# Kernel optimization log

Measured on AMD Instinct MI355X. Metric: run time of the kernel, lower is better.

Reference implementation:

```python
import jax, jax.numpy as jnp
import numpy as np

B, L, D, N, R = 8, 4096, 768, 16, 8

def setup_inputs() -> dict:
    key = jax.random.key(0)
    ks = jax.random.split(key, 12)
    return {
        "x": jax.random.normal(ks[0], (B, L, D), jnp.float32),
        "a_logit": jnp.zeros((N,), jnp.float32),
        "U": jax.random.normal(ks[1], (N, R), jnp.float32) * 0.02,
        "V": jax.random.normal(ks[2], (N, R), jnp.float32) * 0.02,
        "W_in": jax.random.normal(ks[3], (N, D), jnp.float32) * (1.0 / np.sqrt(D)),
        "b_in": jax.random.normal(ks[4], (N,), jnp.float32) * 0.02,
        "W_gate": jax.random.normal(ks[5], (N, D), jnp.float32) * (1.0 / np.sqrt(D)),
        "b_gate": jax.random.normal(ks[6], (N,), jnp.float32) * 0.02,
        "W_out": jax.random.normal(ks[7], (D, N), jnp.float32) * (1.0 / np.sqrt(N)),
        "b_out": jax.random.normal(ks[8], (D,), jnp.float32) * 0.02,
        "W_skip": jax.random.normal(ks[9], (D, D), jnp.float32) * (1.0 / np.sqrt(D)),
        "b_skip": jax.random.normal(ks[10], (D,), jnp.float32) * 0.02,
    }

def reference(x, a_logit, U, V, W_in, b_in, W_gate, b_gate, W_out, b_out, W_skip, b_skip):
    # x: [B, L, D]
    u = jnp.einsum('bld,nd->bln', x, W_in) + b_in            # [B, L, N]
    g = jax.nn.sigmoid(jnp.einsum('bld,nd->bln', x, W_gate) + b_gate)
    a = jax.nn.sigmoid(a_logit)                              # [N]
    lowrank_T = V @ U.T                                      # (U @ V.T).T, [N, N]
    gu = g * u                                               # [B, L, N]

    def step(h, gu_t):
        # h: [B, N]; h_new = a*h + g_t*u_t + h @ lowrank.T
        h = h * a + gu_t + h @ lowrank_T
        return h, h

    h0 = jnp.zeros((x.shape[0], a_logit.shape[0]), x.dtype)
    _, hs = jax.lax.scan(step, h0, jnp.swapaxes(gu, 0, 1))   # hs: [L, B, N]
    hs = jnp.swapaxes(hs, 0, 1)                              # [B, L, N]
    # batched out_proj + skip across all timesteps
    y = jnp.einsum('bln,dn->bld', hs, W_out) + b_out \
        + jnp.einsum('ble,de->bld', x, W_skip) + b_skip
    return y
```

## Files before the change

kernel.cpp:

```cpp
#include <hip/hip_runtime.h>
#include <hip/hip_bf16.h>
#include <math.h>

#define BB 8
#define LL 4096
#define DD 768
#define NN 16
#define RR 8
#define MROWS (BB*LL)
#define KAUG 800
#define CCH 64
#define NCH (LL/CCH)

typedef unsigned int u32;
typedef unsigned short u16;
typedef __attribute__((ext_vector_type(8))) short short8;
typedef __attribute__((ext_vector_type(4))) float f32x4;
typedef __attribute__((ext_vector_type(4))) unsigned short us4;

__device__ __forceinline__ u16 f2bf(float f) {
  u32 u = __float_as_uint(f);
  u32 r = (u + 0x7fffu + ((u >> 16) & 1u)) >> 16;
  return (u16)r;
}

__device__ __forceinline__ void gload_lds16(const void* g, void* l) {
  __builtin_amdgcn_global_load_lds(
      (const __attribute__((address_space(1))) u32*)g,
      (__attribute__((address_space(3))) u32*)l, 16, 0, 0);
}

__global__ void k_prep(const float* __restrict__ a_logit, const float* __restrict__ U,
                       const float* __restrict__ V, const float* __restrict__ b_out,
                       const float* __restrict__ b_skip,
                       float* __restrict__ Mw, float* __restrict__ MCw,
                       float* __restrict__ bsum) {
  __shared__ float cur[256];
  __shared__ float nxt[256];
  int t = threadIdx.x;
  int m = t >> 4, n = t & 15;
  float s = 0.f;
  #pragma unroll
  for (int r = 0; r < RR; r++) s += V[m*RR+r] * U[n*RR+r];
  if (m == n) s += 1.f / (1.f + expf(-a_logit[n]));
  cur[t] = s;
  Mw[t] = s;
  __syncthreads();
  for (int it = 0; it < 6; ++it) {
    float acc = 0.f;
    #pragma unroll
    for (int k = 0; k < 16; k++) acc += cur[m*16+k] * cur[k*16+n];
    nxt[t] = acc;
    __syncthreads();
    cur[t] = nxt[t];
    __syncthreads();
  }
  MCw[t] = cur[t];
  for (int d = t; d < DD; d += 256) bsum[d] = b_out[d] + b_skip[d];
}

__global__ void k_weights(const float* __restrict__ W_skip, const float* __restrict__ W_out,
                          const float* __restrict__ W_in, const float* __restrict__ W_gate,
                          u16* __restrict__ Waug, u16* __restrict__ WinG) {
  int bid = blockIdx.x;
  int t = threadIdx.x;
  if (bid < DD) {
    int d = bid;
    for (int c = t; c < KAUG; c += 256) {
      float v;
      if (c < DD)           v = W_skip[d*DD + c];
      else if (c < DD+NN)   v = W_out[d*NN + (c-DD)];
      else                  v = 0.f;
      Waug[d*KAUG + c] = f2bf(v);
    }
  } else {
    int r = bid - DD;
    const float* Wsrc = (r < NN) ? (W_in + r*DD) : (W_gate + (r-NN)*DD);
    for (int c = t; c < DD; c += 256) WinG[r*DD + c] = f2bf(Wsrc[c]);
  }
}

__global__ void k_convert(const float* __restrict__ x, u16* __restrict__ Xaug) {
  int row  = blockIdx.x * 4 + (threadIdx.x >> 6);
  int lane = threadIdx.x & 63;
  const float4* xr = (const float4*)(x + (long)row * DD);
  u16* xo = Xaug + (long)row * KAUG;
  #pragma unroll
  for (int p = 0; p < 3; p++) {
    int c4 = lane + p*64;
    float4 v = xr[c4];
    us4 o;
    o.x = f2bf(v.x); o.y = f2bf(v.y); o.z = f2bf(v.z); o.w = f2bf(v.w);
    *(us4*)(xo + c4*4) = o;
  }
  if (lane < 4) *(us4*)(xo + 784 + lane*4) = (us4)0;
}

__global__ __launch_bounds__(256) void k_gu(const u16* __restrict__ Xaug,
                                            const u16* __restrict__ WinG,
                                            const float* __restrict__ b_in,
                                            const float* __restrict__ b_gate,
                                            float* __restrict__ gu_T) {
  __shared__ u16 At[128*32];
  __shared__ u16 Bt[32*32];
  int tid = threadIdx.x;
  int wave = tid >> 6, lane = tid & 63;
  int rowbase = blockIdx.x * 128;
  f32x4 acc[2][2] = {};
  for (int it = 0; it < DD/32; ++it) {
    int k0 = it * 32;
    #pragma unroll
    for (int p = 0; p < 2; p++) {
      int c = tid + p*256;
      int r = c >> 2, co = c & 3;
      gload_lds16(Xaug + (long)(rowbase + r)*KAUG + k0 + co*8, At + c*8);
    }
    if (tid < 128) {
      int r = tid >> 2, co = tid & 3;
      gload_lds16(WinG + r*DD + k0 + co*8, Bt + tid*8);
    }
    __syncthreads();
    int l15 = lane & 15, lh = lane >> 4;
    short8 a[2], b[2];
    #pragma unroll
    for (int i = 0; i < 2; i++)
      a[i] = *(const short8*)(At + (wave*32 + i*16 + l15)*32 + lh*8);
    #pragma unroll
    for (int j = 0; j < 2; j++)
      b[j] = *(const short8*)(Bt + (j*16 + l15)*32 + lh*8);
    #pragma unroll
    for (int i = 0; i < 2; i++)
      #pragma unroll
      for (int j = 0; j < 2; j++)
        acc[i][j] = __builtin_amdgcn_mfma_f32_16x16x32_bf16(a[i], b[j], acc[i][j], 0, 0, 0);
    __syncthreads();
  }
  int l15 = lane & 15, lh = lane >> 4;
  float bi = b_in[l15], bg = b_gate[l15];
  #pragma unroll
  for (int i = 0; i < 2; i++) {
    int row0 = rowbase + wave*32 + i*16 + lh*4;
    int b = row0 >> 12;
    int t0 = row0 & 4095;
    float4 o;
    {
      float u0 = acc[i][0][0] + bi, u1 = acc[i][0][1] + bi;
      float u2 = acc[i][0][2] + bi, u3 = acc[i][0][3] + bi;
      float g0 = 1.f/(1.f+__expf(-(acc[i][1][0]+bg)));
      float g1 = 1.f/(1.f+__expf(-(acc[i][1][1]+bg)));
      float g2 = 1.f/(1.f+__expf(-(acc[i][1][2]+bg)));
      float g3 = 1.f/(1.f+__expf(-(acc[i][1][3]+bg)));
      o.x = g0*u0; o.y = g1*u1; o.z = g2*u2; o.w = g3*u3;
    }
    *(float4*)(gu_T + ((long)(b*16 + l15) << 12) + t0) = o;
  }
}

__global__ void k_scan_local(const float* __restrict__ gu_T, const float* __restrict__ Mw,
                             float* __restrict__ cend) {
  int lane = threadIdx.x & 63;
  int grp = lane >> 4, n = lane & 15;
  int cid = blockIdx.x*4 + grp;
  int b = cid >> 6, k = cid & 63;
  float Mcol[16];
  #pragma unroll
  for (int m = 0; m < 16; m++) Mcol[m] = Mw[m*16 + n];
  const float4* g4 = (const float4*)(gu_T + ((long)(b*16 + n) << 12) + k*CCH);
  float gv[CCH];
  #pragma unroll
  for (int q = 0; q < CCH/4; q++) {
    float4 v = g4[q];
    gv[q*4+0]=v.x; gv[q*4+1]=v.y; gv[q*4+2]=v.z; gv[q*4+3]=v.w;
  }
  float h = 0.f;
  #pragma unroll
  for (int t = 0; t < CCH; t++) {
    float hn = gv[t];
    #pragma unroll
    for (int m = 0; m < 16; m++) hn += __shfl(h, m, 16) * Mcol[m];
    h = hn;
  }
  cend[(b*NCH + k)*NN + n] = h;
}

__global__ void k_scan_prefix(const float* __restrict__ cend, const float* __restrict__ MCw,
                              float* __restrict__ Hstart) {
  __shared__ float s[BB*NCH*NN];
  int t = threadIdx.x;
  for (int i = t; i < BB*NCH*NN; i += 256) s[i] = cend[i];
  __syncthreads();
  if (t < 128) {
    int b = t >> 4, n = t & 15;
    float Mcol[16];
    #pragma unroll
    for (int m = 0; m < 16; m++) Mcol[m] = MCw[m*16 + n];
    float h = 0.f;
    for (int k = 0; k < NCH; k++) {
      Hstart[(b*NCH + k)*NN + n] = h;
      float hn = s[(b*NCH + k)*NN + n];
      #pragma unroll
      for (int m = 0; m < 16; m++) hn += __shfl(h, m, 16) * Mcol[m];
      h = hn;
    }
  }
}

__global__ void k_scan_final(const float* __restrict__ gu_T, const float* __restrict__ Mw,
                             const float* __restrict__ Hstart, u16* __restrict__ Xaug) {
  int lane = threadIdx.x & 63;
  int grp = lane >> 4, n = lane & 15;
  int cid = blockIdx.x*4 + grp;
  int b = cid >> 6, k = cid & 63;
  float Mcol[16];
  #pragma unroll
  for (int m = 0; m < 16; m++) Mcol[m] = Mw[m*16 + n];
  const float4* g4 = (const float4*)(gu_T + ((long)(b*16 + n) << 12) + k*CCH);
  float gv[CCH];
  #pragma unroll
  for (int q = 0; q < CCH/4; q++) {
    float4 v = g4[q];
    gv[q*4+0]=v.x; gv[q*4+1]=v.y; gv[q*4+2]=v.z; gv[q*4+3]=v.w;
  }
  float h = Hstart[(b*NCH + k)*NN + n];
  u16* xa = Xaug + ((long)(b*LL) + k*CCH)*KAUG + DD + n;
  #pragma unroll
  for (int t = 0; t < CCH; t++) {
    float hn = gv[t];
    #pragma unroll
    for (int m = 0; m < 16; m++) hn += __shfl(h, m, 16) * Mcol[m];
    h = hn;
    xa[(long)t*KAUG] = f2bf(h);
  }
}

__global__ __launch_bounds__(256) void k_out(const u16* __restrict__ Xaug,
                                             const u16* __restrict__ Waug,
                                             const float* __restrict__ bsum,
                                             float* __restrict__ y) {
  __shared__ u16 At[128*32];
  __shared__ u16 Bt[128*32];
  int tid = threadIdx.x;
  int wave = tid >> 6, lane = tid & 63;
  int wm = wave >> 1, wn = wave & 1;
  int bid = blockIdx.x;
  int swz = (bid & 7) * 192 + (bid >> 3);
  int rowbase = (swz & 255) * 128;
  int colbase = (swz >> 8) * 128;
  f32x4 acc[4][4] = {};
  for (int it = 0; it < KAUG/32; ++it) {
    int k0 = it * 32;
    #pragma unroll
    for (int p = 0; p < 2; p++) {
      int c = tid + p*256;
      int r = c >> 2, co = c & 3;
      gload_lds16(Xaug + (long)(rowbase + r)*KAUG + k0 + co*8, At + c*8);
      gload_lds16(Waug + (long)(colbase + r)*KAUG + k0 + co*8, Bt + c*8);
    }
    __syncthreads();
    int l15 = lane & 15, lh = lane >> 4;
    short8 a[4], b[4];
    #pragma unroll
    for (int i = 0; i < 4; i++)
      a[i] = *(const short8*)(At + (wm*64 + i*16 + l15)*32 + lh*8);
    #pragma unroll
    for (int j = 0; j < 4; j++)
      b[j] = *(const short8*)(Bt + (wn*64 + j*16 + l15)*32 + lh*8);
    #pragma unroll
    for (int i = 0; i < 4; i++)
      #pragma unroll
      for (int j = 0; j < 4; j++)
        acc[i][j] = __builtin_amdgcn_mfma_f32_16x16x32_bf16(a[i], b[j], acc[i][j], 0, 0, 0);
    __syncthreads();
  }
  int l15 = lane & 15, lh = lane >> 4;
  #pragma unroll
  for (int j = 0; j < 4; j++) {
    int col = colbase + wn*64 + j*16 + l15;
    float bs = bsum[col];
    #pragma unroll
    for (int i = 0; i < 4; i++) {
      int row0 = rowbase + wm*64 + i*16 + lh*4;
      #pragma unroll
      for (int r = 0; r < 4; r++)
        y[(long)(row0 + r)*DD + col] = acc[i][j][r] + bs;
    }
  }
}

extern "C" void kernel_launch(void* const* d_in, const int* in_sizes, int n_in,
                              void* d_out, int out_size, void* d_ws, size_t ws_size,
                              hipStream_t stream) {
  (void)in_sizes; (void)n_in; (void)out_size; (void)ws_size;
  const float* x       = (const float*)d_in[0];
  const float* a_logit = (const float*)d_in[1];
  const float* U       = (const float*)d_in[2];
  const float* V       = (const float*)d_in[3];
  const float* W_in    = (const float*)d_in[4];
  const float* b_in    = (const float*)d_in[5];
  const float* W_gate  = (const float*)d_in[6];
  const float* b_gate  = (const float*)d_in[7];
  const float* W_out   = (const float*)d_in[8];
  const float* b_out   = (const float*)d_in[9];
  const float* W_skip  = (const float*)d_in[10];
  const float* b_skip  = (const float*)d_in[11];

  char* ws = (char*)d_ws;
  u16*   Xaug = (u16*)(ws + 0);
  u16*   Waug = (u16*)(ws + 52428800);
  u16*   WinG = (u16*)(ws + 53657600);
  float* gu_T = (float*)(ws + 53706752);
  float* Mw   = (float*)(ws + 55803904);
  float* MCw  = (float*)(ws + 55804928);
  float* cend = (float*)(ws + 55805952);
  float* Hst  = (float*)(ws + 55838720);
  float* bsum = (float*)(ws + 55871488);
  float* y    = (float*)d_out;

  hipLaunchKernelGGL(k_prep,        dim3(1),       dim3(256), 0, stream,
                     a_logit, U, V, b_out, b_skip, Mw, MCw, bsum);
  hipLaunchKernelGGL(k_weights,     dim3(800),     dim3(256), 0, stream,
                     W_skip, W_out, W_in, W_gate, Waug, WinG);
  hipLaunchKernelGGL(k_convert,     dim3(MROWS/4), dim3(256), 0, stream, x, Xaug);
  hipLaunchKernelGGL(k_gu,          dim3(256),     dim3(256), 0, stream,
                     Xaug, WinG, b_in, b_gate, gu_T);
  hipLaunchKernelGGL(k_scan_local,  dim3(128),     dim3(64),  0, stream, gu_T, Mw, cend);
  hipLaunchKernelGGL(k_scan_prefix, dim3(1),       dim3(256), 0, stream, cend, MCw, Hst);
  hipLaunchKernelGGL(k_scan_final,  dim3(128),     dim3(64),  0, stream, gu_T, Mw, Hst, Xaug);
  hipLaunchKernelGGL(k_out,         dim3(1536),    dim3(256), 0, stream,
                     Xaug, Waug, bsum, y);
}
```

Before: 334.2 us.

## Fuse x-to-bf16 conversion into GEMM loads and drop augmented X buffer

Result: no change. 330.4 us (-1.1%).

```diff
diff --git a/kernel.cpp b/kernel.cpp
--- a/kernel.cpp
+++ b/kernel.cpp
@@ -17,11 +17,17 @@
 typedef __attribute__((ext_vector_type(8))) short short8;
 typedef __attribute__((ext_vector_type(4))) float f32x4;
 typedef __attribute__((ext_vector_type(4))) unsigned short us4;
+typedef __attribute__((ext_vector_type(4))) u32 u32x4;
 
 __device__ __forceinline__ u16 f2bf(float f) {
   u32 u = __float_as_uint(f);
   u32 r = (u + 0x7fffu + ((u >> 16) & 1u)) >> 16;
   return (u16)r;
+}
+
+__device__ __forceinline__ u32 pk2bf(float a, float b) {
+  __hip_bfloat162 h = __float22bfloat162_rn(make_float2(a, b));
+  return *reinterpret_cast<u32*>(&h);
 }
 
 __device__ __forceinline__ void gload_lds16(const void* g, void* l) {
@@ -80,23 +86,7 @@
   }
 }
 
-__global__ void k_convert(const float* __restrict__ x, u16* __restrict__ Xaug) {
-  int row  = blockIdx.x * 4 + (threadIdx.x >> 6);
-  int lane = threadIdx.x & 63;
-  const float4* xr = (const float4*)(x + (long)row * DD);
-  u16* xo = Xaug + (long)row * KAUG;
-  #pragma unroll
-  for (int p = 0; p < 3; p++) {
-    int c4 = lane + p*64;
-    float4 v = xr[c4];
-    us4 o;
-    o.x = f2bf(v.x); o.y = f2bf(v.y); o.z = f2bf(v.z); o.w = f2bf(v.w);
-    *(us4*)(xo + c4*4) = o;
-  }
-  if (lane < 4) *(us4*)(xo + 784 + lane*4) = (us4)0;
-}
-
-__global__ __launch_bounds__(256) void k_gu(const u16* __restrict__ Xaug,
+__global__ __launch_bounds__(256) void k_gu(const float* __restrict__ x,
                                             const u16* __restrict__ WinG,
                                             const float* __restrict__ b_in,
                                             const float* __restrict__ b_gate,
@@ -106,18 +96,25 @@
   int tid = threadIdx.x;
   int wave = tid >> 6, lane = tid & 63;
   int rowbase = blockIdx.x * 128;
+  int r = tid >> 1, ch = tid & 1;
+  const float* xrow = x + (long)(rowbase + r)*DD + ch*16;
   f32x4 acc[2][2] = {};
   for (int it = 0; it < DD/32; ++it) {
     int k0 = it * 32;
-    #pragma unroll
-    for (int p = 0; p < 2; p++) {
-      int c = tid + p*256;
-      int r = c >> 2, co = c & 3;
-      gload_lds16(Xaug + (long)(rowbase + r)*KAUG + k0 + co*8, At + c*8);
+    {
+      const float4* xp = (const float4*)(xrow + k0);
+      float4 f0 = xp[0], f1 = xp[1], f2 = xp[2], f3 = xp[3];
+      u32x4 lo, hi;
+      lo.x = pk2bf(f0.x,f0.y); lo.y = pk2bf(f0.z,f0.w);
+      lo.z = pk2bf(f1.x,f1.y); lo.w = pk2bf(f1.z,f1.w);
+      hi.x = pk2bf(f2.x,f2.y); hi.y = pk2bf(f2.z,f2.w);
+      hi.z = pk2bf(f3.x,f3.y); hi.w = pk2bf(f3.z,f3.w);
+      *(u32x4*)(At + r*32 + ch*16)     = lo;
+      *(u32x4*)(At + r*32 + ch*16 + 8) = hi;
     }
     if (tid < 128) {
-      int r = tid >> 2, co = tid & 3;
-      gload_lds16(WinG + r*DD + k0 + co*8, Bt + tid*8);
+      int br = tid >> 2, co = tid & 3;
+      gload_lds16(WinG + br*DD + k0 + co*8, Bt + tid*8);
     }
     __syncthreads();
     int l15 = lane & 15, lh = lane >> 4;
@@ -206,7 +203,7 @@
 }
 
 __global__ void k_scan_final(const float* __restrict__ gu_T, const float* __restrict__ Mw,
-                             const float* __restrict__ Hstart, u16* __restrict__ Xaug) {
+                             const float* __restrict__ Hstart, u16* __restrict__ hs) {
   int lane = threadIdx.x & 63;
   int grp = lane >> 4, n = lane & 15;
   int cid = blockIdx.x*4 + grp;
@@ -222,18 +219,19 @@
     gv[q*4+0]=v.x; gv[q*4+1]=v.y; gv[q*4+2]=v.z; gv[q*4+3]=v.w;
   }
   float h = Hstart[(b*NCH + k)*NN + n];
-  u16* xa = Xaug + ((long)(b*LL) + k*CCH)*KAUG + DD + n;
+  u16* hp = hs + ((long)(b*LL) + k*CCH)*NN + n;
   #pragma unroll
   for (int t = 0; t < CCH; t++) {
     float hn = gv[t];
     #pragma unroll
     for (int m = 0; m < 16; m++) hn += __shfl(h, m, 16) * Mcol[m];
     h = hn;
-    xa[(long)t*KAUG] = f2bf(h);
-  }
-}
-
-__global__ __launch_bounds__(256) void k_out(const u16* __restrict__ Xaug,
+    hp[(long)t*NN] = f2bf(h);
+  }
+}
+
+__global__ __launch_bounds__(256) void k_out(const float* __restrict__ x,
+                                             const u16* __restrict__ hs,
                                              const u16* __restrict__ Waug,
                                              const float* __restrict__ bsum,
                                              float* __restrict__ y) {
@@ -242,19 +240,39 @@
   int tid = threadIdx.x;
   int wave = tid >> 6, lane = tid & 63;
   int wm = wave >> 1, wn = wave & 1;
-  int bid = blockIdx.x;
-  int swz = (bid & 7) * 192 + (bid >> 3);
-  int rowbase = (swz & 255) * 128;
-  int colbase = (swz >> 8) * 128;
+  int rowbase = blockIdx.x * 128;
+  int colbase = blockIdx.y * 128;
+  int r = tid >> 1, ch = tid & 1;
+  const float* xrow = x + (long)(rowbase + r)*DD + ch*16;
   f32x4 acc[4][4] = {};
-  for (int it = 0; it < KAUG/32; ++it) {
+  for (int it = 0; it < 25; ++it) {
     int k0 = it * 32;
     #pragma unroll
     for (int p = 0; p < 2; p++) {
-      int c = tid + p*256;
-      int r = c >> 2, co = c & 3;
-      gload_lds16(Xaug + (long)(rowbase + r)*KAUG + k0 + co*8, At + c*8);
-      gload_lds16(Waug + (long)(colbase + r)*KAUG + k0 + co*8, Bt + c*8);
+      int cc = tid + p*256;
+      int br = cc >> 2, bco = cc & 3;
+      gload_lds16(Waug + (long)(colbase + br)*KAUG + k0 + bco*8, Bt + cc*8);
+    }
+    if (it < 24) {
+      const float4* xp = (const float4*)(xrow + k0);
+      float4 f0 = xp[0], f1 = xp[1], f2 = xp[2], f3 = xp[3];
+      u32x4 lo, hi;
+      lo.x = pk2bf(f0.x,f0.y); lo.y = pk2bf(f0.z,f0.w);
+      lo.z = pk2bf(f1.x,f1.y); lo.w = pk2bf(f1.z,f1.w);
+      hi.x = pk2bf(f2.x,f2.y); hi.y = pk2bf(f2.z,f2.w);
+      hi.z = pk2bf(f3.x,f3.y); hi.w = pk2bf(f3.z,f3.w);
+      *(u32x4*)(At + r*32 + ch*16)     = lo;
+      *(u32x4*)(At + r*32 + ch*16 + 8) = hi;
+    } else {
+      if (ch == 0) {
+        const u32x4* hp = (const u32x4*)(hs + (long)(rowbase + r)*NN);
+        *(u32x4*)(At + r*32)     = hp[0];
+        *(u32x4*)(At + r*32 + 8) = hp[1];
+      } else {
+        u32x4 z = (u32x4)0;
+        *(u32x4*)(At + r*32 + 16) = z;
+        *(u32x4*)(At + r*32 + 24) = z;
+      }
     }
     __syncthreads();
     int l15 = lane & 15, lh = lane >> 4;
@@ -281,8 +299,8 @@
     for (int i = 0; i < 4; i++) {
       int row0 = rowbase + wm*64 + i*16 + lh*4;
       #pragma unroll
-      for (int r = 0; r < 4; r++)
-        y[(long)(row0 + r)*DD + col] = acc[i][j][r] + bs;
+      for (int rr = 0; rr < 4; rr++)
+        y[(long)(row0 + rr)*DD + col] = acc[i][j][rr] + bs;
     }
   }
 }
@@ -305,27 +323,26 @@
   const float* b_skip  = (const float*)d_in[11];
 
   char* ws = (char*)d_ws;
-  u16*   Xaug = (u16*)(ws + 0);
-  u16*   Waug = (u16*)(ws + 52428800);
-  u16*   WinG = (u16*)(ws + 53657600);
-  float* gu_T = (float*)(ws + 53706752);
-  float* Mw   = (float*)(ws + 55803904);
-  float* MCw  = (float*)(ws + 55804928);
-  float* cend = (float*)(ws + 55805952);
-  float* Hst  = (float*)(ws + 55838720);
-  float* bsum = (float*)(ws + 55871488);
+  u16*   Waug = (u16*)(ws + 0);
+  u16*   WinG = (u16*)(ws + 1228800);
+  float* gu_T = (float*)(ws + 1277952);
+  u16*   hs   = (u16*)(ws + 3375104);
+  float* Mw   = (float*)(ws + 4423680);
+  float* MCw  = (float*)(ws + 4424704);
+  float* cend = (float*)(ws + 4425728);
+  float* Hst  = (float*)(ws + 4458496);
+  float* bsum = (float*)(ws + 4491264);
   float* y    = (float*)d_out;
 
-  hipLaunchKernelGGL(k_prep,        dim3(1),       dim3(256), 0, stream,
+  hipLaunchKernelGGL(k_prep,        dim3(1),      dim3(256), 0, stream,
                      a_logit, U, V, b_out, b_skip, Mw, MCw, bsum);
-  hipLaunchKernelGGL(k_weights,     dim3(800),     dim3(256), 0, stream,
+  hipLaunchKernelGGL(k_weights,     dim3(800),    dim3(256), 0, stream,
                      W_skip, W_out, W_in, W_gate, Waug, WinG);
-  hipLaunchKernelGGL(k_convert,     dim3(MROWS/4), dim3(256), 0, stream, x, Xaug);
-  hipLaunchKernelGGL(k_gu,          dim3(256),     dim3(256), 0, stream,
-                     Xaug, WinG, b_in, b_gate, gu_T);
-  hipLaunchKernelGGL(k_scan_local,  dim3(128),     dim3(64),  0, stream, gu_T, Mw, cend);
-  hipLaunchKernelGGL(k_scan_prefix, dim3(1),       dim3(256), 0, stream, cend, MCw, Hst);
-  hipLaunchKernelGGL(k_scan_final,  dim3(128),     dim3(64),  0, stream, gu_T, Mw, Hst, Xaug);
-  hipLaunchKernelGGL(k_out,         dim3(1536),    dim3(256), 0, stream,
-                     Xaug, Waug, bsum, y);
-}
+  hipLaunchKernelGGL(k_gu,          dim3(256),    dim3(256), 0, stream,
+                     x, WinG, b_in, b_gate, gu_T);
+  hipLaunchKernelGGL(k_scan_local,  dim3(128),    dim3(64),  0, stream, gu_T, Mw, cend);
+  hipLaunchKernelGGL(k_scan_prefix, dim3(1),      dim3(256), 0, stream, cend, MCw, Hst);
+  hipLaunchKernelGGL(k_scan_final,  dim3(128),    dim3(64),  0, stream, gu_T, Mw, Hst, hs);
+  hipLaunchKernelGGL(k_out,         dim3(256, 6), dim3(256), 0, stream,
+                     x, hs, Waug, bsum, y);
+}
```
